# Kernel optimization log

Hardware: AMD Instinct MI355X
Metric: run time of the kernel (lower is better)

## Reference

```python
import jax, jax.numpy as jnp
import numpy as np

N, E, F_IN, HID, H, NC, G = 50000, 800000, 128, 64, 4, 64, 128
EPS_BN = 1e-5


def setup_inputs() -> dict:
    key = jax.random.key(0)
    ks = jax.random.split(key, 32)
    inp = {}
    inp['x'] = jax.random.normal(ks[0], (N, F_IN), dtype=jnp.float32)
    inp['edge_index'] = jax.random.randint(ks[1], (2, E), 0, N, dtype=jnp.int32)
    inp['batch'] = jnp.sort(jax.random.randint(ks[2], (N,), 0, G, dtype=jnp.int32))
    dims = [(F_IN, HID, H, True), (HID * H, HID, H, True), (HID * H, NC, 1, False)]
    k = 3
    for li, (fin, c, h, concat) in enumerate(dims):
        out_flat = c * h if concat else c
        inp[f'W{li}'] = jax.random.normal(ks[k], (fin, h * c), dtype=jnp.float32) * (1.0 / np.sqrt(fin)); k += 1
        inp[f'asrc{li}'] = jax.random.normal(ks[k], (h, c), dtype=jnp.float32) * 0.1; k += 1
        inp[f'adst{li}'] = jax.random.normal(ks[k], (h, c), dtype=jnp.float32) * 0.1; k += 1
        inp[f'b{li}'] = jnp.zeros((out_flat,), dtype=jnp.float32)
        inp[f'gamma{li}'] = jnp.ones((out_flat,), dtype=jnp.float32)
        inp[f'beta{li}'] = jnp.zeros((out_flat,), dtype=jnp.float32)
    return inp


def gat_layer(x, src, dst, W, asrc, adst, b, heads, out_ch, concat):
    n = x.shape[0]
    h = (x @ W).reshape(n, heads, out_ch)                      # [N,H,C]
    a_s = jnp.sum(h * asrc, axis=-1)                           # [N,H]
    a_d = jnp.sum(h * adst, axis=-1)                           # [N,H]
    e = jax.nn.leaky_relu(a_s[src] + a_d[dst], 0.2)            # [E',H]
    m = jax.ops.segment_max(e, dst, num_segments=n)            # per-target max
    e = jnp.exp(e - m[dst])
    s = jax.ops.segment_sum(e, dst, num_segments=n)
    alpha = e / (s[dst] + 1e-16)                               # softmax over in-edges
    msg = alpha[:, :, None] * h[src]                           # [E',H,C]
    out = jax.ops.segment_sum(msg, dst, num_segments=n)        # [N,H,C]
    out = out.reshape(n, heads * out_ch) if concat else out.mean(axis=1)
    return out + b


def batchnorm(x, gamma, beta):
    mu = x.mean(axis=0)
    var = x.var(axis=0)  # biased, as torch BN training-mode
    return (x - mu) * jax.lax.rsqrt(var + EPS_BN) * gamma + beta


def reference(x, edge_index, batch, W0, asrc0, adst0, b0, gamma0, beta0,
              W1, asrc1, adst1, b1, gamma1, beta1,
              W2, asrc2, adst2, b2, gamma2, beta2):
    n = x.shape[0]
    loop = jnp.arange(n, dtype=edge_index.dtype)
    src = jnp.concatenate([edge_index[0], loop])  # add self loops (PyG default)
    dst = jnp.concatenate([edge_index[1], loop])
    layers = [(W0, asrc0, adst0, b0, gamma0, beta0, H, HID, True),
              (W1, asrc1, adst1, b1, gamma1, beta1, H, HID, True),
              (W2, asrc2, adst2, b2, gamma2, beta2, 1, NC, False)]
    xs = []
    for (W, asrc, adst, b, gamma, beta, heads, oc, concat) in layers:
        x = jax.nn.elu(gat_layer(x, src, dst, W, asrc, adst, b, heads, oc, concat))
        x = batchnorm(x, gamma, beta)
        xs.append(x)
    x_pool = jnp.concatenate([jax.ops.segment_sum(xx, batch, num_segments=G) for xx in xs], axis=1)
    return (x_pool, jnp.concatenate(xs, axis=1))
```

## Files before the change

### kernel.cpp

```cpp
#include <hip/hip_runtime.h>
#include <math.h>

#define N_NODES 50000
#define NUM_E   800000
#define E_TOT   (NUM_E + N_NODES)
#define M_PAD   50048
#define NGRAPH  128
#define XS_COLS 576
#define EPS_BN  1e-5f

static inline int ceil_div(int a, int b) { return (a + b - 1) / b; }

typedef __attribute__((ext_vector_type(8))) short short8;
typedef __attribute__((ext_vector_type(4))) float f32x4;

__device__ __forceinline__ float bf2f(ushort u) {
    union { unsigned int i; float f; } v; v.i = ((unsigned int)u) << 16; return v.f;
}
__device__ __forceinline__ ushort f2bf(float f) {
    union { float f; unsigned int i; } v; v.f = f;
    unsigned int r = v.i + 0x7FFF + ((v.i >> 16) & 1);
    return (ushort)(r >> 16);
}
__device__ __forceinline__ float lrelu(float l) { return l > 0.f ? l : 0.2f * l; }

__global__ __launch_bounds__(256)
void prep_all(const float* __restrict__ x, const float* __restrict__ W0,
              const float* __restrict__ W1, const float* __restrict__ W2,
              ushort* __restrict__ Abf0, ushort* __restrict__ Wt0,
              ushort* __restrict__ Wt1, ushort* __restrict__ Wt2)
{
    int i = blockIdx.x * 256 + threadIdx.x;
    const int NX4 = N_NODES * 128 / 4;
    if (i < NX4) {
        float4 v = reinterpret_cast<const float4*>(x)[i];
        ushort4 o;
        o.x = f2bf(v.x); o.y = f2bf(v.y); o.z = f2bf(v.z); o.w = f2bf(v.w);
        reinterpret_cast<ushort4*>(Abf0)[i] = o;
        return;
    }
    int j = i - NX4;
    if (j < 256 * 128) { Wt0[j] = f2bf(W0[(size_t)(j % 128) * 256 + (j / 128)]); return; }
    j -= 256 * 128;
    if (j < 256 * 256) { Wt1[j] = f2bf(W1[(size_t)(j % 256) * 256 + (j / 256)]); return; }
    j -= 256 * 256;
    if (j < 64 * 256)  { Wt2[j] = f2bf(W2[(size_t)(j % 256) * 64 + (j / 256)]); }
}

__global__ __launch_bounds__(512)
void gemm_bf16_w(const ushort* __restrict__ A, int lda,
                 const ushort* __restrict__ Bt, int ldb,
                 ushort* __restrict__ C, int M, int K,
                 const float* __restrict__ asrc, const float* __restrict__ adst,
                 float* __restrict__ a_s, float* __restrict__ a_d)
{
    __shared__ __align__(16) ushort As[128][64 + 8];
    __shared__ __align__(16) ushort Bs[256][64 + 8];
    const int tid = threadIdx.x;
    const int lane = tid & 63;
    const int w = tid >> 6;
    const int m0 = blockIdx.x * 128;

    f32x4 acc[16] = {};

    for (int k0 = 0; k0 < K; k0 += 64) {
#pragma unroll
        for (int j = 0; j < 2; ++j) {
            int c = tid + j * 512;
            int r = c >> 3, cc = (c & 7) * 8;
            short8 v = *reinterpret_cast<const short8*>(A + (size_t)(m0 + r) * lda + k0 + cc);
            *reinterpret_cast<short8*>(&As[r][cc]) = v;
        }
#pragma unroll
        for (int j = 0; j < 4; ++j) {
            int c = tid + j * 512;
            int r = c >> 3, cc = (c & 7) * 8;
            short8 v = *reinterpret_cast<const short8*>(Bt + (size_t)r * ldb + k0 + cc);
            *reinterpret_cast<short8*>(&Bs[r][cc]) = v;
        }
        __syncthreads();
#pragma unroll
        for (int kc = 0; kc < 64; kc += 32) {
            short8 a = *reinterpret_cast<const short8*>(&As[w * 16 + (lane & 15)][kc + (lane >> 4) * 8]);
#pragma unroll
            for (int nf = 0; nf < 16; ++nf) {
                short8 b = *reinterpret_cast<const short8*>(&Bs[nf * 16 + (lane & 15)][kc + (lane >> 4) * 8]);
                acc[nf] = __builtin_amdgcn_mfma_f32_16x16x32_bf16(a, b, acc[nf], 0, 0, 0);
            }
        }
        __syncthreads();
    }

    const int mbase = m0 + w * 16 + (lane >> 4) * 4;
#pragma unroll
    for (int r = 0; r < 4; ++r) {
        int m = mbase + r;
        if (m < M) {
#pragma unroll
            for (int nf = 0; nf < 16; ++nf)
                C[(size_t)m * 256 + nf * 16 + (lane & 15)] = f2bf(acc[nf][r]);
        }
    }

    float asl[16], adl[16];
#pragma unroll
    for (int nf = 0; nf < 16; ++nf) {
        int col = nf * 16 + (lane & 15);
        asl[nf] = asrc[col];
        adl[nf] = adst[col];
    }
#pragma unroll
    for (int r = 0; r < 4; ++r) {
        float ps[4] = {0.f, 0.f, 0.f, 0.f};
        float pd[4] = {0.f, 0.f, 0.f, 0.f};
#pragma unroll
        for (int nf = 0; nf < 16; ++nf) {
            int h = nf >> 2;
            ps[h] = fmaf(acc[nf][r], asl[nf], ps[h]);
            pd[h] = fmaf(acc[nf][r], adl[nf], pd[h]);
        }
#pragma unroll
        for (int h = 0; h < 4; ++h) {
#pragma unroll
            for (int o = 1; o < 16; o <<= 1) {
                ps[h] += __shfl_xor(ps[h], o, 64);
                pd[h] += __shfl_xor(pd[h], o, 64);
            }
        }
        int m = mbase + r;
        if ((lane & 15) == 0 && m < M) {
#pragma unroll
            for (int h = 0; h < 4; ++h) {
                a_s[(size_t)m * 4 + h] = ps[h];
                a_d[(size_t)m * 4 + h] = pd[h];
            }
        }
    }
}

template<int BM, int BN, int BK, int H>
__global__ __launch_bounds__(256)
void gemm_bf16(const ushort* __restrict__ A, int lda,
               const ushort* __restrict__ Bt, int ldb,
               ushort* __restrict__ C, int ldc, int M, int K,
               const float* __restrict__ asrc, const float* __restrict__ adst,
               float* __restrict__ a_s, float* __restrict__ a_d)
{
    static_assert(BM == 128 && BN == 64 && BK == 64, "tuned variant");
    __shared__ __align__(16) ushort As[BM][BK + 8];
    __shared__ __align__(16) ushort Bs[BN][BK + 8];
    const int tid = threadIdx.x;
    const int lane = tid & 63;
    const int w = tid >> 6;
    const int m0 = blockIdx.x * BM;
    const int n0 = blockIdx.y * BN;

    f32x4 acc[2][4] = {};

    for (int k0 = 0; k0 < K; k0 += BK) {
#pragma unroll
        for (int j = 0; j < 4; ++j) {
            int c = tid + j * 256;
            int r = c >> 3, cc = (c & 7) * 8;
            short8 v = *reinterpret_cast<const short8*>(A + (size_t)(m0 + r) * lda + k0 + cc);
            *reinterpret_cast<short8*>(&As[r][cc]) = v;
        }
#pragma unroll
        for (int j = 0; j < 2; ++j) {
            int c = tid + j * 256;
            int r = c >> 3, cc = (c & 7) * 8;
            short8 v = *reinterpret_cast<const short8*>(Bt + (size_t)(n0 + r) * ldb + k0 + cc);
            *reinterpret_cast<short8*>(&Bs[r][cc]) = v;
        }
        __syncthreads();
#pragma unroll
        for (int kc = 0; kc < BK; kc += 32) {
            short8 a[2], b[4];
#pragma unroll
            for (int mf = 0; mf < 2; ++mf)
                a[mf] = *reinterpret_cast<const short8*>(&As[w * 32 + mf * 16 + (lane & 15)][kc + (lane >> 4) * 8]);
#pragma unroll
            for (int nf = 0; nf < 4; ++nf)
                b[nf] = *reinterpret_cast<const short8*>(&Bs[nf * 16 + (lane & 15)][kc + (lane >> 4) * 8]);
#pragma unroll
            for (int mf = 0; mf < 2; ++mf)
#pragma unroll
                for (int nf = 0; nf < 4; ++nf)
                    acc[mf][nf] = __builtin_amdgcn_mfma_f32_16x16x32_bf16(a[mf], b[nf], acc[mf][nf], 0, 0, 0);
        }
        __syncthreads();
    }

#pragma unroll
    for (int mf = 0; mf < 2; ++mf) {
        int mbase = m0 + w * 32 + mf * 16 + (lane >> 4) * 4;
#pragma unroll
        for (int r = 0; r < 4; ++r) {
            int m = mbase + r;
            if (m < M) {
#pragma unroll
                for (int nf = 0; nf < 4; ++nf)
                    C[(size_t)m * ldc + n0 + nf * 16 + (lane & 15)] = f2bf(acc[mf][nf][r]);
            }
        }
    }

    const int hd = blockIdx.y;
    float asl[4], adl[4];
#pragma unroll
    for (int nf = 0; nf < 4; ++nf) {
        int col = n0 + nf * 16 + (lane & 15);
        asl[nf] = asrc[col];
        adl[nf] = adst[col];
    }
#pragma unroll
    for (int mf = 0; mf < 2; ++mf) {
#pragma unroll
        for (int r = 0; r < 4; ++r) {
            float ps = 0.f, pd = 0.f;
#pragma unroll
            for (int nf = 0; nf < 4; ++nf) {
                ps = fmaf(acc[mf][nf][r], asl[nf], ps);
                pd = fmaf(acc[mf][nf][r], adl[nf], pd);
            }
#pragma unroll
            for (int o = 1; o < 16; o <<= 1) {
                ps += __shfl_xor(ps, o, 64);
                pd += __shfl_xor(pd, o, 64);
            }
            int m = m0 + w * 32 + mf * 16 + (lane >> 4) * 4 + r;
            if ((lane & 15) == 0 && m < M) {
                a_s[(size_t)m * H + hd] = ps;
                a_d[(size_t)m * H + hd] = pd;
            }
        }
    }
}

template<int H, int C>
__global__ __launch_bounds__(256)
void gat_fused(const int* __restrict__ offs, const int* __restrict__ ssrc,
               const float* __restrict__ a_s, const float* __restrict__ a_d,
               const ushort* __restrict__ hf, const float* __restrict__ bias,
               float* __restrict__ out, int ldo)
{
    constexpr int V = (H * C) / 64;
    __shared__ float alsh[4][64 * H];
    const int lane = threadIdx.x & 63;
    const int wv = threadIdx.x >> 6;
    const int dst = blockIdx.x * 4 + wv;
    if (dst >= N_NODES) return;
    const int e0 = offs[dst], e1 = offs[dst + 1];
    const int deg = e1 - e0;
    const int hd = (lane * V) / C;

    float ad[H];
    if constexpr (H == 4) {
        float4 v = *reinterpret_cast<const float4*>(a_d + (size_t)dst * 4);
        ad[0] = v.x; ad[1] = v.y; ad[2] = v.z; ad[3] = v.w;
    } else ad[0] = a_d[dst];

    float acc[V];
#pragma unroll
    for (int k = 0; k < V; ++k) acc[k] = 0.f;

    if (deg <= 64) {
        int e = e0 + lane;
        bool act = e < e1;
        int s = ssrc[act ? e : e0];
        float l[H], mx[H], sm[H];
        if constexpr (H == 4) {
            float4 v = *reinterpret_cast<const float4*>(a_s + (size_t)s * 4);
            l[0] = lrelu(v.x + ad[0]); l[1] = lrelu(v.y + ad[1]);
            l[2] = lrelu(v.z + ad[2]); l[3] = lrelu(v.w + ad[3]);
        } else l[0] = lrelu(a_s[s] + ad[0]);
#pragma unroll
        for (int t = 0; t < H; ++t) {
            mx[t] = act ? l[t] : -INFINITY;
#pragma unroll
            for (int o = 1; o < 64; o <<= 1) mx[t] = fmaxf(mx[t], __shfl_xor(mx[t], o, 64));
            sm[t] = act ? __expf(l[t] - mx[t]) : 0.f;
#pragma unroll
            for (int o = 1; o < 64; o <<= 1) sm[t] += __shfl_xor(sm[t], o, 64);
        }
        if constexpr (H == 4) {
            float4 av;
            av.x = act ? __expf(l[0] - mx[0]) / (sm[0] + 1e-16f) : 0.f;
            av.y = act ? __expf(l[1] - mx[1]) / (sm[1] + 1e-16f) : 0.f;
            av.z = act ? __expf(l[2] - mx[2]) / (sm[2] + 1e-16f) : 0.f;
            av.w = act ? __expf(l[3] - mx[3]) / (sm[3] + 1e-16f) : 0.f;
            *reinterpret_cast<float4*>(&alsh[wv][lane * 4]) = av;
        } else {
            alsh[wv][lane] = act ? __expf(l[0] - mx[0]) / (sm[0] + 1e-16f) : 0.f;
        }
        const ushort* hlane = hf + (size_t)lane * V;
        int e2 = e0;
        for (; e2 + 7 < e1; e2 += 8) {
            int base = e2 - e0;
            int sj[8]; float al[8];
#pragma unroll
            for (int j = 0; j < 8; ++j) {
                sj[j] = __shfl(s, base + j, 64);
                al[j] = alsh[wv][(base + j) * H + hd];
            }
            if constexpr (V == 4) {
                ushort4 hv[8];
#pragma unroll
                for (int j = 0; j < 8; ++j)
                    hv[j] = *reinterpret_cast<const ushort4*>(hlane + (size_t)sj[j] * (H * C));
#pragma unroll
                for (int j = 0; j < 8; ++j) {
                    acc[0] = fmaf(al[j], bf2f(hv[j].x), acc[0]);
                    acc[1] = fmaf(al[j], bf2f(hv[j].y), acc[1]);
                    acc[2] = fmaf(al[j], bf2f(hv[j].z), acc[2]);
                    acc[3] = fmaf(al[j], bf2f(hv[j].w), acc[3]);
                }
            } else {
                ushort hv[8];
#pragma unroll
                for (int j = 0; j < 8; ++j)
                    hv[j] = hlane[(size_t)sj[j] * (H * C)];
#pragma unroll
                for (int j = 0; j < 8; ++j)
                    acc[0] = fmaf(al[j], bf2f(hv[j]), acc[0]);
            }
        }
        for (; e2 < e1; ++e2) {
            int base = e2 - e0;
            int s0 = __shfl(s, base, 64);
            float al0 = alsh[wv][base * H + hd];
            if constexpr (V == 4) {
                ushort4 h0 = *reinterpret_cast<const ushort4*>(hlane + (size_t)s0 * (H * C));
                acc[0] = fmaf(al0, bf2f(h0.x), acc[0]); acc[1] = fmaf(al0, bf2f(h0.y), acc[1]);
                acc[2] = fmaf(al0, bf2f(h0.z), acc[2]); acc[3] = fmaf(al0, bf2f(h0.w), acc[3]);
            } else {
                acc[0] = fmaf(al0, bf2f(hlane[(size_t)s0 * (H * C)]), acc[0]);
            }
        }
    } else {
        float mx[H], sm[H];
#pragma unroll
        for (int t = 0; t < H; ++t) mx[t] = -INFINITY;
        for (int e = e0 + lane; e < e1; e += 64) {
            int s = ssrc[e];
            float asv[H];
            if constexpr (H == 4) {
                float4 v = *reinterpret_cast<const float4*>(a_s + (size_t)s * 4);
                asv[0] = v.x; asv[1] = v.y; asv[2] = v.z; asv[3] = v.w;
            } else asv[0] = a_s[s];
#pragma unroll
            for (int t = 0; t < H; ++t) mx[t] = fmaxf(mx[t], lrelu(asv[t] + ad[t]));
        }
#pragma unroll
        for (int t = 0; t < H; ++t)
#pragma unroll
            for (int o = 1; o < 64; o <<= 1) mx[t] = fmaxf(mx[t], __shfl_xor(mx[t], o, 64));
#pragma unroll
        for (int t = 0; t < H; ++t) sm[t] = 0.f;
        for (int e = e0 + lane; e < e1; e += 64) {
            int s = ssrc[e];
            float asv[H];
            if constexpr (H == 4) {
                float4 v = *reinterpret_cast<const float4*>(a_s + (size_t)s * 4);
                asv[0] = v.x; asv[1] = v.y; asv[2] = v.z; asv[3] = v.w;
            } else asv[0] = a_s[s];
#pragma unroll
            for (int t = 0; t < H; ++t) sm[t] += __expf(lrelu(asv[t] + ad[t]) - mx[t]);
        }
#pragma unroll
        for (int t = 0; t < H; ++t)
#pragma unroll
            for (int o = 1; o < 64; o <<= 1) sm[t] += __shfl_xor(sm[t], o, 64);

        float mxl = mx[0], sml = sm[0], adl = ad[0];
#pragma unroll
        for (int t = 1; t < H; ++t) {
            mxl = (hd == t) ? mx[t] : mxl;
            sml = (hd == t) ? sm[t] : sml;
            adl = (hd == t) ? ad[t] : adl;
        }
        const float invl = 1.f / (sml + 1e-16f);
        for (int e = e0; e < e1; ++e) {
            int s0 = ssrc[e];
            float al0 = __expf(lrelu(a_s[(size_t)s0 * H + hd] + adl) - mxl) * invl;
            if constexpr (V == 4) {
                ushort4 h0 = *reinterpret_cast<const ushort4*>(hf + (size_t)s0 * (H * C) + lane * 4);
                acc[0] = fmaf(al0, bf2f(h0.x), acc[0]); acc[1] = fmaf(al0, bf2f(h0.y), acc[1]);
                acc[2] = fmaf(al0, bf2f(h0.z), acc[2]); acc[3] = fmaf(al0, bf2f(h0.w), acc[3]);
            } else {
                acc[0] = fmaf(al0, bf2f(hf[(size_t)s0 * (H * C) + lane]), acc[0]);
            }
        }
    }

    if constexpr (V == 4) {
        float t0 = acc[0] + bias[lane * 4 + 0];
        float t1 = acc[1] + bias[lane * 4 + 1];
        float t2 = acc[2] + bias[lane * 4 + 2];
        float t3 = acc[3] + bias[lane * 4 + 3];
        float4 v;
        v.x = t0 > 0.f ? t0 : (expf(t0) - 1.f);
        v.y = t1 > 0.f ? t1 : (expf(t1) - 1.f);
        v.z = t2 > 0.f ? t2 : (expf(t2) - 1.f);
        v.w = t3 > 0.f ? t3 : (expf(t3) - 1.f);
        *reinterpret_cast<float4*>(&out[(size_t)dst * ldo + lane * 4]) = v;
    } else {
        float t0 = acc[0] + bias[lane];
        out[(size_t)dst * ldo + lane] = t0 > 0.f ? t0 : (expf(t0) - 1.f);
    }
}

__global__ void edge_count(const int* __restrict__ ei, int* __restrict__ counts)
{
    int i = blockIdx.x * blockDim.x + threadIdx.x;
    if (i >= E_TOT) return;
    int dst = (i < NUM_E) ? ei[NUM_E + i] : (i - NUM_E);
    atomicAdd(&counts[dst], 1);
}

__global__ void edge_scatter(const int* __restrict__ ei, int* __restrict__ cursor,
                             int* __restrict__ ssrc)
{
    int i = blockIdx.x * blockDim.x + threadIdx.x;
    if (i >= E_TOT) return;
    int src, dst;
    if (i < NUM_E) { src = ei[i]; dst = ei[NUM_E + i]; }
    else           { src = dst = i - NUM_E; }
    int pos = atomicAdd(&cursor[dst], 1);
    ssrc[pos] = src;
}

__global__ void scan_block(const int* __restrict__ in, int n,
                           int* __restrict__ incl, int* __restrict__ bsum)
{
    __shared__ int sh[256];
    int tid = threadIdx.x;
    int i = blockIdx.x * 256 + tid;
    int v = (i < n) ? in[i] : 0;
    sh[tid] = v;
    __syncthreads();
    for (int o = 1; o < 256; o <<= 1) {
        int t = (tid >= o) ? sh[tid - o] : 0;
        __syncthreads();
        sh[tid] += t;
        __syncthreads();
    }
    if (i < n) incl[i] = sh[tid];
    if (tid == 255) bsum[blockIdx.x] = sh[255];
}

__global__ void scan_sums(int* __restrict__ bsum, int nb)
{
    __shared__ int sh[256];
    int tid = threadIdx.x;
    int v = (tid < nb) ? bsum[tid] : 0;
    sh[tid] = v;
    __syncthreads();
    for (int o = 1; o < 256; o <<= 1) {
        int t = (tid >= o) ? sh[tid - o] : 0;
        __syncthreads();
        sh[tid] += t;
        __syncthreads();
    }
    if (tid < nb) bsum[tid] = sh[tid] - v;
}

__global__ void scan_final(const int* __restrict__ incl, const int* __restrict__ in,
                           const int* __restrict__ bsum, int n,
                           int* __restrict__ offs, int* __restrict__ cursor)
{
    int i = blockIdx.x * 256 + threadIdx.x;
    if (i >= n) return;
    int excl = incl[i] - in[i] + bsum[i / 256];
    offs[i] = excl;
    cursor[i] = excl;
    if (i == n - 1) offs[n] = incl[i] + bsum[i / 256];
}

template<int OF>
__global__ __launch_bounds__(256)
void bn_stats(const float* __restrict__ x, int ldx, float* __restrict__ part)
{
    constexpr int RP = 256 / OF;
    const int tid = threadIdx.x;
    const int col = tid % OF;
    const int rsub = tid / OF;
    float s = 0.f, s2 = 0.f;
    for (int r = blockIdx.x * RP + rsub; r < N_NODES; r += gridDim.x * RP) {
        float v = x[(size_t)r * ldx + col];
        s += v;
        s2 = fmaf(v, v, s2);
    }
    if constexpr (RP > 1) {
        __shared__ float sh[2][256];
        sh[0][tid] = s; sh[1][tid] = s2;
        __syncthreads();
        if (rsub == 0) {
#pragma unroll
            for (int j = 1; j < RP; ++j) { s += sh[0][col + j * OF]; s2 += sh[1][col + j * OF]; }
        }
    }
    if (rsub == 0) {
        part[(size_t)blockIdx.x * 2 * OF + col] = s;
        part[(size_t)blockIdx.x * 2 * OF + OF + col] = s2;
    }
}

template<int OF>
__global__ void bn_finalize(const float* __restrict__ part, const float* __restrict__ gamma,
                            const float* __restrict__ beta, float* __restrict__ ss)
{
    int c = threadIdx.x;
    if (c >= OF) return;
    float s = 0.f, s2 = 0.f;
    for (int b = 0; b < 256; ++b) {
        s += part[(size_t)b * 2 * OF + c];
        s2 += part[(size_t)b * 2 * OF + OF + c];
    }
    float mean = s / (float)N_NODES;
    float var = s2 / (float)N_NODES - mean * mean;
    float inv = rsqrtf(var + EPS_BN);
    float sc = inv * gamma[c];
    ss[c] = sc;
    ss[OF + c] = beta[c] - mean * sc;
}

template<int OF, bool WB>
__global__ __launch_bounds__(256)
void bn_apply_pool(float* __restrict__ x, int ldx, const float* __restrict__ ss,
                   ushort* __restrict__ xb, int ldxb,
                   const int* __restrict__ batch, float* __restrict__ pool, int poff)
{
    const int tid = threadIdx.x;
    if constexpr (OF == 256) {
        const int c = tid;
        const int r0 = blockIdx.x * 16;
        const float sc = ss[c], sh = ss[OF + c];
        float psum = 0.f;
        int curg = batch[r0];
#pragma unroll
        for (int i = 0; i < 16; ++i) {
            int r = r0 + i;
            int g = batch[r];
            if (g != curg) {
                atomicAdd(&pool[(size_t)curg * XS_COLS + poff + c], psum);
                psum = 0.f; curg = g;
            }
            float v = fmaf(x[(size_t)r * ldx + c], sc, sh);
            x[(size_t)r * ldx + c] = v;
            if constexpr (WB) xb[(size_t)r * ldxb + c] = f2bf(v);
            psum += v;
        }
        atomicAdd(&pool[(size_t)curg * XS_COLS + poff + c], psum);
    } else {
        const int c = tid & 63;
        const int rsub = tid >> 6;
        const int r0 = blockIdx.x * 16;
        const float sc = ss[c], sh = ss[OF + c];
        float psum = 0.f;
        int curg = batch[r0 + rsub];
#pragma unroll
        for (int i = 0; i < 4; ++i) {
            int r = r0 + rsub + i * 4;
            int g = batch[r];
            if (g != curg) {
                atomicAdd(&pool[(size_t)curg * XS_COLS + poff + c], psum);
                psum = 0.f; curg = g;
            }
            float v = fmaf(x[(size_t)r * ldx + c], sc, sh);
            x[(size_t)r * ldx + c] = v;
            if constexpr (WB) xb[(size_t)r * ldxb + c] = f2bf(v);
            psum += v;
        }
        atomicAdd(&pool[(size_t)curg * XS_COLS + poff + c], psum);
    }
}

extern "C" void kernel_launch(void* const* d_in, const int* in_sizes, int n_in,
                              void* d_out, int out_size, void* d_ws, size_t ws_size,
                              hipStream_t stream)
{
    const float* x     = (const float*)d_in[0];
    const int*   ei    = (const int*)d_in[1];
    const int*   batch = (const int*)d_in[2];
    const float* W[3]    = {(const float*)d_in[3],  (const float*)d_in[9],  (const float*)d_in[15]};
    const float* asrc[3] = {(const float*)d_in[4],  (const float*)d_in[10], (const float*)d_in[16]};
    const float* adst[3] = {(const float*)d_in[5],  (const float*)d_in[11], (const float*)d_in[17]};
    const float* bia[3]  = {(const float*)d_in[6],  (const float*)d_in[12], (const float*)d_in[18]};
    const float* gam[3]  = {(const float*)d_in[7],  (const float*)d_in[13], (const float*)d_in[19]};
    const float* bet[3]  = {(const float*)d_in[8],  (const float*)d_in[14], (const float*)d_in[20]};

    char* wp = (char*)d_ws;
    auto alloc = [&](size_t bytes) -> void* {
        void* p = (void*)wp;
        wp += (bytes + 255) & ~(size_t)255;
        return p;
    };
    ushort* hbf   = (ushort*)alloc((size_t)N_NODES * 256 * 2);
    ushort* Abf0  = (ushort*)alloc((size_t)M_PAD * 128 * 2);
    ushort* AbfA  = (ushort*)alloc((size_t)M_PAD * 256 * 2);
    float*  a_s   = (float*)alloc((size_t)N_NODES * 4 * 4);
    float*  a_d   = (float*)alloc((size_t)N_NODES * 4 * 4);
    int*    counts = (int*)alloc((size_t)N_NODES * 4);
    int*    offs   = (int*)alloc((size_t)(N_NODES + 1) * 4);
    int*    cursor = (int*)alloc((size_t)N_NODES * 4);
    int*    incl   = (int*)alloc((size_t)N_NODES * 4);
    int*    bsums  = (int*)alloc(1024);
    int*    ssrc   = (int*)alloc((size_t)E_TOT * 4);
    float*  bnpart = (float*)alloc((size_t)256 * 2 * 256 * 4);
    float*  bnss   = (float*)alloc(2 * 256 * 4);
    ushort* Wt0    = (ushort*)alloc(256 * 128 * 2);
    ushort* Wt1    = (ushort*)alloc(256 * 256 * 2);
    ushort* Wt2    = (ushort*)alloc(64 * 256 * 2);

    float* pool = (float*)d_out;
    float* xs   = pool + (size_t)NGRAPH * XS_COLS;

    hipMemsetAsync(counts, 0, (size_t)N_NODES * 4, stream);
    hipMemsetAsync(pool, 0, (size_t)NGRAPH * XS_COLS * 4, stream);
    edge_count<<<ceil_div(E_TOT, 256), 256, 0, stream>>>(ei, counts);
    const int NSB = ceil_div(N_NODES, 256);
    scan_block<<<NSB, 256, 0, stream>>>(counts, N_NODES, incl, bsums);
    scan_sums<<<1, 256, 0, stream>>>(bsums, NSB);
    scan_final<<<NSB, 256, 0, stream>>>(incl, counts, bsums, N_NODES, offs, cursor);
    edge_scatter<<<ceil_div(E_TOT, 256), 256, 0, stream>>>(ei, cursor, ssrc);
    const int PREP_ITEMS = N_NODES * 128 / 4 + 256 * 128 + 256 * 256 + 64 * 256;
    prep_all<<<ceil_div(PREP_ITEMS, 256), 256, 0, stream>>>(x, W[0], W[1], W[2], Abf0, Wt0, Wt1, Wt2);

    const int NW = ceil_div(N_NODES, 4);
    const int NMB = ceil_div(N_NODES, 128);
    const int NBA = N_NODES / 16;

    {
        gemm_bf16_w<<<NMB, 512, 0, stream>>>(Abf0, 128, Wt0, 128, hbf, N_NODES, 128,
                                             asrc[0], adst[0], a_s, a_d);
        gat_fused<4, 64><<<NW, 256, 0, stream>>>(offs, ssrc, a_s, a_d, hbf, bia[0], xs + 0, XS_COLS);
        bn_stats<256><<<256, 256, 0, stream>>>(xs + 0, XS_COLS, bnpart);
        bn_finalize<256><<<1, 256, 0, stream>>>(bnpart, gam[0], bet[0], bnss);
        bn_apply_pool<256, true><<<NBA, 256, 0, stream>>>(xs + 0, XS_COLS, bnss, AbfA, 256,
                                                          batch, pool, 0);
    }
    {
        gemm_bf16_w<<<NMB, 512, 0, stream>>>(AbfA, 256, Wt1, 256, hbf, N_NODES, 256,
                                             asrc[1], adst[1], a_s, a_d);
        gat_fused<4, 64><<<NW, 256, 0, stream>>>(offs, ssrc, a_s, a_d, hbf, bia[1], xs + 256, XS_COLS);
        bn_stats<256><<<256, 256, 0, stream>>>(xs + 256, XS_COLS, bnpart);
        bn_finalize<256><<<1, 256, 0, stream>>>(bnpart, gam[1], bet[1], bnss);
        bn_apply_pool<256, true><<<NBA, 256, 0, stream>>>(xs + 256, XS_COLS, bnss, AbfA, 256,
                                                          batch, pool, 256);
    }
    {
        dim3 grid(NMB, 1);
        gemm_bf16<128, 64, 64, 1><<<grid, 256, 0, stream>>>(AbfA, 256, Wt2, 256, hbf, 64, N_NODES, 256,
                                                            asrc[2], adst[2], a_s, a_d);
        gat_fused<1, 64><<<NW, 256, 0, stream>>>(offs, ssrc, a_s, a_d, hbf, bia[2], xs + 512, XS_COLS);
        bn_stats<64><<<256, 256, 0, stream>>>(xs + 512, XS_COLS, bnpart);
        bn_finalize<64><<<1, 64, 0, stream>>>(bnpart, gam[2], bet[2], bnss);
        bn_apply_pool<64, false><<<NBA, 256, 0, stream>>>(xs + 512, XS_COLS, bnss, nullptr, 0,
                                                          batch, pool, 512);
    }
}
```

Before: 554.8 us.

## Process two destination nodes per wavefront and fuse x bf16 conversion into GEMM

The GAT aggregation kernel now assigns each half-wavefront (32 lanes) to one destination node. Each lane handles two edges in the softmax stage and gathers 8 bf16 features per source row with short8 loads. Source indices are staged in shared memory instead of being broadcast by shuffles. Separately, the fp32-to-bf16 conversion of the input features moves into the first GEMM's tile load, which drops a conversion pass and its buffer. The trade-offs are a larger per-lane working set, and edges for one node are gathered by fewer lanes.

```diff
diff --git a/kernel.cpp b/kernel.cpp
--- a/kernel.cpp
+++ b/kernel.cpp
@@ -25,21 +25,11 @@
 __device__ __forceinline__ float lrelu(float l) { return l > 0.f ? l : 0.2f * l; }
 
 __global__ __launch_bounds__(256)
-void prep_all(const float* __restrict__ x, const float* __restrict__ W0,
-              const float* __restrict__ W1, const float* __restrict__ W2,
-              ushort* __restrict__ Abf0, ushort* __restrict__ Wt0,
-              ushort* __restrict__ Wt1, ushort* __restrict__ Wt2)
-{
-    int i = blockIdx.x * 256 + threadIdx.x;
-    const int NX4 = N_NODES * 128 / 4;
-    if (i < NX4) {
-        float4 v = reinterpret_cast<const float4*>(x)[i];
-        ushort4 o;
-        o.x = f2bf(v.x); o.y = f2bf(v.y); o.z = f2bf(v.z); o.w = f2bf(v.w);
-        reinterpret_cast<ushort4*>(Abf0)[i] = o;
-        return;
-    }
-    int j = i - NX4;
+void prep_w(const float* __restrict__ W0, const float* __restrict__ W1,
+            const float* __restrict__ W2,
+            ushort* __restrict__ Wt0, ushort* __restrict__ Wt1, ushort* __restrict__ Wt2)
+{
+    int j = blockIdx.x * 256 + threadIdx.x;
     if (j < 256 * 128) { Wt0[j] = f2bf(W0[(size_t)(j % 128) * 256 + (j / 128)]); return; }
     j -= 256 * 128;
     if (j < 256 * 256) { Wt1[j] = f2bf(W1[(size_t)(j % 256) * 256 + (j / 256)]); return; }
@@ -47,8 +37,9 @@
     if (j < 64 * 256)  { Wt2[j] = f2bf(W2[(size_t)(j % 256) * 64 + (j / 256)]); }
 }
 
+template<bool AF32>
 __global__ __launch_bounds__(512)
-void gemm_bf16_w(const ushort* __restrict__ A, int lda,
+void gemm_bf16_w(const void* __restrict__ Av, int lda,
                  const ushort* __restrict__ Bt, int ldb,
                  ushort* __restrict__ C, int M, int K,
                  const float* __restrict__ asrc, const float* __restrict__ adst,
@@ -68,8 +59,19 @@
         for (int j = 0; j < 2; ++j) {
             int c = tid + j * 512;
             int r = c >> 3, cc = (c & 7) * 8;
-            short8 v = *reinterpret_cast<const short8*>(A + (size_t)(m0 + r) * lda + k0 + cc);
-            *reinterpret_cast<short8*>(&As[r][cc]) = v;
+            if constexpr (AF32) {
+                const float* Af = (const float*)Av;
+                int m = m0 + r; if (m >= M) m = M - 1;
+                float4 v0 = *reinterpret_cast<const float4*>(Af + (size_t)m * lda + k0 + cc);
+                float4 v1 = *reinterpret_cast<const float4*>(Af + (size_t)m * lda + k0 + cc + 4);
+                short8 v = {(short)f2bf(v0.x), (short)f2bf(v0.y), (short)f2bf(v0.z), (short)f2bf(v0.w),
+                            (short)f2bf(v1.x), (short)f2bf(v1.y), (short)f2bf(v1.z), (short)f2bf(v1.w)};
+                *reinterpret_cast<short8*>(&As[r][cc]) = v;
+            } else {
+                const ushort* Ab = (const ushort*)Av;
+                short8 v = *reinterpret_cast<const short8*>(Ab + (size_t)(m0 + r) * lda + k0 + cc);
+                *reinterpret_cast<short8*>(&As[r][cc]) = v;
+            }
         }
 #pragma unroll
         for (int j = 0; j < 4; ++j) {
@@ -239,20 +241,24 @@
 
 template<int H, int C>
 __global__ __launch_bounds__(256)
-void gat_fused(const int* __restrict__ offs, const int* __restrict__ ssrc,
-               const float* __restrict__ a_s, const float* __restrict__ a_d,
-               const ushort* __restrict__ hf, const float* __restrict__ bias,
-               float* __restrict__ out, int ldo)
-{
-    constexpr int V = (H * C) / 64;
-    __shared__ float alsh[4][64 * H];
-    const int lane = threadIdx.x & 63;
-    const int wv = threadIdx.x >> 6;
-    const int dst = blockIdx.x * 4 + wv;
+void gat_fused2(const int* __restrict__ offs, const int* __restrict__ ssrc,
+                const float* __restrict__ a_s, const float* __restrict__ a_d,
+                const ushort* __restrict__ hf, const float* __restrict__ bias,
+                float* __restrict__ out, int ldo)
+{
+    constexpr int V = (H * C) / 32;
+    __shared__ float alsh[4][2][64 * H];
+    __shared__ int   ssh[4][2][64];
+    const int tid = threadIdx.x;
+    const int lane = tid & 63;
+    const int wv = tid >> 6;
+    const int half = lane >> 5;
+    const int ll = lane & 31;
+    const int dst = blockIdx.x * 8 + wv * 2 + half;
     if (dst >= N_NODES) return;
     const int e0 = offs[dst], e1 = offs[dst + 1];
     const int deg = e1 - e0;
-    const int hd = (lane * V) / C;
+    const int hd = (ll * V) / C;
 
     float ad[H];
     if constexpr (H == 4) {
@@ -265,83 +271,104 @@
     for (int k = 0; k < V; ++k) acc[k] = 0.f;
 
     if (deg <= 64) {
-        int e = e0 + lane;
-        bool act = e < e1;
-        int s = ssrc[act ? e : e0];
-        float l[H], mx[H], sm[H];
+        const bool a0 = ll < deg;
+        const bool a1 = 32 + ll < deg;
+        const int s0 = ssrc[e0 + (a0 ? ll : 0)];
+        const int s1 = ssrc[e0 + (a1 ? 32 + ll : 0)];
+        float l0[H], l1[H], mx[H], sm[H];
         if constexpr (H == 4) {
-            float4 v = *reinterpret_cast<const float4*>(a_s + (size_t)s * 4);
-            l[0] = lrelu(v.x + ad[0]); l[1] = lrelu(v.y + ad[1]);
-            l[2] = lrelu(v.z + ad[2]); l[3] = lrelu(v.w + ad[3]);
-        } else l[0] = lrelu(a_s[s] + ad[0]);
+            float4 v0 = *reinterpret_cast<const float4*>(a_s + (size_t)s0 * 4);
+            float4 v1 = *reinterpret_cast<const float4*>(a_s + (size_t)s1 * 4);
+            l0[0] = lrelu(v0.x + ad[0]); l0[1] = lrelu(v0.y + ad[1]);
+            l0[2] = lrelu(v0.z + ad[2]); l0[3] = lrelu(v0.w + ad[3]);
+            l1[0] = lrelu(v1.x + ad[0]); l1[1] = lrelu(v1.y + ad[1]);
+            l1[2] = lrelu(v1.z + ad[2]); l1[3] = lrelu(v1.w + ad[3]);
+        } else {
+            l0[0] = lrelu(a_s[s0] + ad[0]);
+            l1[0] = lrelu(a_s[s1] + ad[0]);
+        }
 #pragma unroll
         for (int t = 0; t < H; ++t) {
-            mx[t] = act ? l[t] : -INFINITY;
-#pragma unroll
-            for (int o = 1; o < 64; o <<= 1) mx[t] = fmaxf(mx[t], __shfl_xor(mx[t], o, 64));
-            sm[t] = act ? __expf(l[t] - mx[t]) : 0.f;
-#pragma unroll
-            for (int o = 1; o < 64; o <<= 1) sm[t] += __shfl_xor(sm[t], o, 64);
-        }
-        if constexpr (H == 4) {
-            float4 av;
-            av.x = act ? __expf(l[0] - mx[0]) / (sm[0] + 1e-16f) : 0.f;
-            av.y = act ? __expf(l[1] - mx[1]) / (sm[1] + 1e-16f) : 0.f;
-            av.z = act ? __expf(l[2] - mx[2]) / (sm[2] + 1e-16f) : 0.f;
-            av.w = act ? __expf(l[3] - mx[3]) / (sm[3] + 1e-16f) : 0.f;
-            *reinterpret_cast<float4*>(&alsh[wv][lane * 4]) = av;
-        } else {
-            alsh[wv][lane] = act ? __expf(l[0] - mx[0]) / (sm[0] + 1e-16f) : 0.f;
-        }
-        const ushort* hlane = hf + (size_t)lane * V;
-        int e2 = e0;
-        for (; e2 + 7 < e1; e2 += 8) {
-            int base = e2 - e0;
-            int sj[8]; float al[8];
-#pragma unroll
-            for (int j = 0; j < 8; ++j) {
-                sj[j] = __shfl(s, base + j, 64);
-                al[j] = alsh[wv][(base + j) * H + hd];
-            }
-            if constexpr (V == 4) {
-                ushort4 hv[8];
-#pragma unroll
-                for (int j = 0; j < 8; ++j)
-                    hv[j] = *reinterpret_cast<const ushort4*>(hlane + (size_t)sj[j] * (H * C));
-#pragma unroll
-                for (int j = 0; j < 8; ++j) {
-                    acc[0] = fmaf(al[j], bf2f(hv[j].x), acc[0]);
-                    acc[1] = fmaf(al[j], bf2f(hv[j].y), acc[1]);
-                    acc[2] = fmaf(al[j], bf2f(hv[j].z), acc[2]);
-                    acc[3] = fmaf(al[j], bf2f(hv[j].w), acc[3]);
+            float m = a0 ? l0[t] : -INFINITY;
+            if (a1) m = fmaxf(m, l1[t]);
+#pragma unroll
+            for (int o = 1; o < 32; o <<= 1) m = fmaxf(m, __shfl_xor(m, o, 64));
+            mx[t] = m;
+            float s = (a0 ? __expf(l0[t] - m) : 0.f) + (a1 ? __expf(l1[t] - m) : 0.f);
+#pragma unroll
+            for (int o = 1; o < 32; o <<= 1) s += __shfl_xor(s, o, 64);
+            sm[t] = s;
+        }
+        float inv[H];
+#pragma unroll
+        for (int t = 0; t < H; ++t) inv[t] = 1.f / (sm[t] + 1e-16f);
+        if (a0) {
+            ssh[wv][half][ll] = s0;
+            if constexpr (H == 4) {
+                float4 av = {__expf(l0[0] - mx[0]) * inv[0], __expf(l0[1] - mx[1]) * inv[1],
+                             __expf(l0[2] - mx[2]) * inv[2], __expf(l0[3] - mx[3]) * inv[3]};
+                *reinterpret_cast<float4*>(&alsh[wv][half][ll * 4]) = av;
+            } else alsh[wv][half][ll] = __expf(l0[0] - mx[0]) * inv[0];
+        }
+        if (a1) {
+            ssh[wv][half][32 + ll] = s1;
+            if constexpr (H == 4) {
+                float4 av = {__expf(l1[0] - mx[0]) * inv[0], __expf(l1[1] - mx[1]) * inv[1],
+                             __expf(l1[2] - mx[2]) * inv[2], __expf(l1[3] - mx[3]) * inv[3]};
+                *reinterpret_cast<float4*>(&alsh[wv][half][(32 + ll) * 4]) = av;
+            } else alsh[wv][half][32 + ll] = __expf(l1[0] - mx[0]) * inv[0];
+        }
+
+        const ushort* hlane = hf + (size_t)ll * V;
+        int j = 0;
+        for (; j + 3 < deg; j += 4) {
+            int sj[4]; float al[4];
+#pragma unroll
+            for (int k = 0; k < 4; ++k) {
+                sj[k] = ssh[wv][half][j + k];
+                al[k] = alsh[wv][half][(j + k) * H + hd];
+            }
+            if constexpr (V == 8) {
+                short8 hv[4];
+#pragma unroll
+                for (int k = 0; k < 4; ++k)
+                    hv[k] = *reinterpret_cast<const short8*>(hlane + (size_t)sj[k] * (H * C));
+#pragma unroll
+                for (int k = 0; k < 4; ++k)
+#pragma unroll
+                    for (int i = 0; i < 8; ++i)
+                        acc[i] = fmaf(al[k], bf2f((ushort)hv[k][i]), acc[i]);
+            } else {
+                ushort2 hv[4];
+#pragma unroll
+                for (int k = 0; k < 4; ++k)
+                    hv[k] = *reinterpret_cast<const ushort2*>(hlane + (size_t)sj[k] * (H * C));
+#pragma unroll
+                for (int k = 0; k < 4; ++k) {
+                    acc[0] = fmaf(al[k], bf2f(hv[k].x), acc[0]);
+                    acc[1] = fmaf(al[k], bf2f(hv[k].y), acc[1]);
                 }
+            }
+        }
+        for (; j < deg; ++j) {
+            int sj = ssh[wv][half][j];
+            float al = alsh[wv][half][j * H + hd];
+            if constexpr (V == 8) {
+                short8 hv = *reinterpret_cast<const short8*>(hlane + (size_t)sj * (H * C));
+#pragma unroll
+                for (int i = 0; i < 8; ++i)
+                    acc[i] = fmaf(al, bf2f((ushort)hv[i]), acc[i]);
             } else {
-                ushort hv[8];
-#pragma unroll
-                for (int j = 0; j < 8; ++j)
-                    hv[j] = hlane[(size_t)sj[j] * (H * C)];
-#pragma unroll
-                for (int j = 0; j < 8; ++j)
-                    acc[0] = fmaf(al[j], bf2f(hv[j]), acc[0]);
-            }
-        }
-        for (; e2 < e1; ++e2) {
-            int base = e2 - e0;
-            int s0 = __shfl(s, base, 64);
-            float al0 = alsh[wv][base * H + hd];
-            if constexpr (V == 4) {
-                ushort4 h0 = *reinterpret_cast<const ushort4*>(hlane + (size_t)s0 * (H * C));
-                acc[0] = fmaf(al0, bf2f(h0.x), acc[0]); acc[1] = fmaf(al0, bf2f(h0.y), acc[1]);
-                acc[2] = fmaf(al0, bf2f(h0.z), acc[2]); acc[3] = fmaf(al0, bf2f(h0.w), acc[3]);
-            } else {
-                acc[0] = fmaf(al0, bf2f(hlane[(size_t)s0 * (H * C)]), acc[0]);
+                ushort2 hv = *reinterpret_cast<const ushort2*>(hlane + (size_t)sj * (H * C));
+                acc[0] = fmaf(al, bf2f(hv.x), acc[0]);
+                acc[1] = fmaf(al, bf2f(hv.y), acc[1]);
             }
         }
     } else {
         float mx[H], sm[H];
 #pragma unroll
         for (int t = 0; t < H; ++t) mx[t] = -INFINITY;
-        for (int e = e0 + lane; e < e1; e += 64) {
+        for (int e = e0 + ll; e < e1; e += 32) {
             int s = ssrc[e];
             float asv[H];
             if constexpr (H == 4) {
@@ -354,10 +381,10 @@
 #pragma unroll
         for (int t = 0; t < H; ++t)
 #pragma unroll
-            for (int o = 1; o < 64; o <<= 1) mx[t] = fmaxf(mx[t], __shfl_xor(mx[t], o, 64));
+            for (int o = 1; o < 32; o <<= 1) mx[t] = fmaxf(mx[t], __shfl_xor(mx[t], o, 64));
 #pragma unroll
         for (int t = 0; t < H; ++t) sm[t] = 0.f;
-        for (int e = e0 + lane; e < e1; e += 64) {
+        for (int e = e0 + ll; e < e1; e += 32) {
             int s = ssrc[e];
             float asv[H];
             if constexpr (H == 4) {
@@ -370,7 +397,7 @@
 #pragma unroll
         for (int t = 0; t < H; ++t)
 #pragma unroll
-            for (int o = 1; o < 64; o <<= 1) sm[t] += __shfl_xor(sm[t], o, 64);
+            for (int o = 1; o < 32; o <<= 1) sm[t] += __shfl_xor(sm[t], o, 64);
 
         float mxl = mx[0], sml = sm[0], adl = ad[0];
 #pragma unroll
@@ -380,33 +407,37 @@
             adl = (hd == t) ? ad[t] : adl;
         }
         const float invl = 1.f / (sml + 1e-16f);
+        const ushort* hlane = hf + (size_t)ll * V;
         for (int e = e0; e < e1; ++e) {
             int s0 = ssrc[e];
             float al0 = __expf(lrelu(a_s[(size_t)s0 * H + hd] + adl) - mxl) * invl;
-            if constexpr (V == 4) {
-                ushort4 h0 = *reinterpret_cast<const ushort4*>(hf + (size_t)s0 * (H * C) + lane * 4);
-                acc[0] = fmaf(al0, bf2f(h0.x), acc[0]); acc[1] = fmaf(al0, bf2f(h0.y), acc[1]);
-                acc[2] = fmaf(al0, bf2f(h0.z), acc[2]); acc[3] = fmaf(al0, bf2f(h0.w), acc[3]);
+            if constexpr (V == 8) {
+                short8 hv = *reinterpret_cast<const short8*>(hlane + (size_t)s0 * (H * C));
+#pragma unroll
+                for (int i = 0; i < 8; ++i)
+                    acc[i] = fmaf(al0, bf2f((ushort)hv[i]), acc[i]);
             } else {
-                acc[0] = fmaf(al0, bf2f(hf[(size_t)s0 * (H * C) + lane]), acc[0]);
-            }
-        }
-    }
-
-    if constexpr (V == 4) {
-        float t0 = acc[0] + bias[lane * 4 + 0];
-        float t1 = acc[1] + bias[lane * 4 + 1];
-        float t2 = acc[2] + bias[lane * 4 + 2];
-        float t3 = acc[3] + bias[lane * 4 + 3];
-        float4 v;
-        v.x = t0 > 0.f ? t0 : (expf(t0) - 1.f);
-        v.y = t1 > 0.f ? t1 : (expf(t1) - 1.f);
-        v.z = t2 > 0.f ? t2 : (expf(t2) - 1.f);
-        v.w = t3 > 0.f ? t3 : (expf(t3) - 1.f);
-        *reinterpret_cast<float4*>(&out[(size_t)dst * ldo + lane * 4]) = v;
+                ushort2 hv = *reinterpret_cast<const ushort2*>(hlane + (size_t)s0 * (H * C));
+                acc[0] = fmaf(al0, bf2f(hv.x), acc[0]);
+                acc[1] = fmaf(al0, bf2f(hv.y), acc[1]);
+            }
+        }
+    }
+
+    float res[V];
+#pragma unroll
+    for (int i = 0; i < V; ++i) {
+        float t = acc[i] + bias[ll * V + i];
+        res[i] = t > 0.f ? t : (expf(t) - 1.f);
+    }
+    if constexpr (V == 8) {
+        float4 v0 = {res[0], res[1], res[2], res[3]};
+        float4 v1 = {res[4], res[5], res[6], res[7]};
+        *reinterpret_cast<float4*>(&out[(size_t)dst * ldo + ll * 8 + 0]) = v0;
+        *reinterpret_cast<float4*>(&out[(size_t)dst * ldo + ll * 8 + 4]) = v1;
     } else {
-        float t0 = acc[0] + bias[lane];
-        out[(size_t)dst * ldo + lane] = t0 > 0.f ? t0 : (expf(t0) - 1.f);
+        float2 v = {res[0], res[1]};
+        *reinterpret_cast<float2*>(&out[(size_t)dst * ldo + ll * 2]) = v;
     }
 }
 
@@ -597,7 +628,6 @@
         return p;
     };
     ushort* hbf   = (ushort*)alloc((size_t)N_NODES * 256 * 2);
-    ushort* Abf0  = (ushort*)alloc((size_t)M_PAD * 128 * 2);
     ushort* AbfA  = (ushort*)alloc((size_t)M_PAD * 256 * 2);
     float*  a_s   = (float*)alloc((size_t)N_NODES * 4 * 4);
     float*  a_d   = (float*)alloc((size_t)N_NODES * 4 * 4);
@@ -624,26 +654,26 @@
     scan_sums<<<1, 256, 0, stream>>>(bsums, NSB);
     scan_final<<<NSB, 256, 0, stream>>>(incl, counts, bsums, N_NODES, offs, cursor);
     edge_scatter<<<ceil_div(E_TOT, 256), 256, 0, stream>>>(ei, cursor, ssrc);
-    const int PREP_ITEMS = N_NODES * 128 / 4 + 256 * 128 + 256 * 256 + 64 * 256;
-    prep_all<<<ceil_div(PREP_ITEMS, 256), 256, 0, stream>>>(x, W[0], W[1], W[2], Abf0, Wt0, Wt1, Wt2);
-
-    const int NW = ceil_div(N_NODES, 4);
+    const int PREP_ITEMS = 256 * 128 + 256 * 256 + 64 * 256;
+    prep_w<<<ceil_div(PREP_ITEMS, 256), 256, 0, stream>>>(W[0], W[1], W[2], Wt0, Wt1, Wt2);
+
+    const int NW2 = ceil_div(N_NODES, 8);
     const int NMB = ceil_div(N_NODES, 128);
     const int NBA = N_NODES / 16;
 
     {
-        gemm_bf16_w<<<NMB, 512, 0, stream>>>(Abf0, 128, Wt0, 128, hbf, N_NODES, 128,
-                                             asrc[0], adst[0], a_s, a_d);
-        gat_fused<4, 64><<<NW, 256, 0, stream>>>(offs, ssrc, a_s, a_d, hbf, bia[0], xs + 0, XS_COLS);
+        gemm_bf16_w<true><<<NMB, 512, 0, stream>>>(x, 128, Wt0, 128, hbf, N_NODES, 128,
+                                                   asrc[0], adst[0], a_s, a_d);
+        gat_fused2<4, 64><<<NW2, 256, 0, stream>>>(offs, ssrc, a_s, a_d, hbf, bia[0], xs + 0, XS_COLS);
         bn_stats<256><<<256, 256, 0, stream>>>(xs + 0, XS_COLS, bnpart);
         bn_finalize<256><<<1, 256, 0, stream>>>(bnpart, gam[0], bet[0], bnss);
         bn_apply_pool<256, true><<<NBA, 256, 0, stream>>>(xs + 0, XS_COLS, bnss, AbfA, 256,
                                                           batch, pool, 0);
     }
     {
-        gemm_bf16_w<<<NMB, 512, 0, stream>>>(AbfA, 256, Wt1, 256, hbf, N_NODES, 256,
-                                             asrc[1], adst[1], a_s, a_d);
-        gat_fused<4, 64><<<NW, 256, 0, stream>>>(offs, ssrc, a_s, a_d, hbf, bia[1], xs + 256, XS_COLS);
+        gemm_bf16_w<false><<<NMB, 512, 0, stream>>>(AbfA, 256, Wt1, 256, hbf, N_NODES, 256,
+                                                    asrc[1], adst[1], a_s, a_d);
+        gat_fused2<4, 64><<<NW2, 256, 0, stream>>>(offs, ssrc, a_s, a_d, hbf, bia[1], xs + 256, XS_COLS);
         bn_stats<256><<<256, 256, 0, stream>>>(xs + 256, XS_COLS, bnpart);
         bn_finalize<256><<<1, 256, 0, stream>>>(bnpart, gam[1], bet[1], bnss);
         bn_apply_pool<256, true><<<NBA, 256, 0, stream>>>(xs + 256, XS_COLS, bnss, AbfA, 256,
@@ -653,7 +683,7 @@
         dim3 grid(NMB, 1);
         gemm_bf16<128, 64, 64, 1><<<grid, 256, 0, stream>>>(AbfA, 256, Wt2, 256, hbf, 64, N_NODES, 256,
                                                             asrc[2], adst[2], a_s, a_d);
-        gat_fused<1, 64><<<NW, 256, 0, stream>>>(offs, ssrc, a_s, a_d, hbf, bia[2], xs + 512, XS_COLS);
+        gat_fused2<1, 64><<<NW2, 256, 0, stream>>>(offs, ssrc, a_s, a_d, hbf, bia[2], xs + 512, XS_COLS);
         bn_stats<64><<<256, 256, 0, stream>>>(xs + 512, XS_COLS, bnpart);
         bn_finalize<64><<<1, 64, 0, stream>>>(bnpart, gam[2], bet[2], bnss);
         bn_apply_pool<64, false><<<NBA, 256, 0, stream>>>(xs + 512, XS_COLS, bnss, nullptr, 0,
```

After: 532.8 us. -4.0%, faster.
